# Performance work log

Hardware: AMD Instinct MI355X
Metric: run time of the kernel (lower is better)

The kernel has to match this reference:

```python
import jax, jax.numpy as jnp
import numpy as np

IN_SHAPE = (128, 128, 128)   # (d, w, h)
RES_SCALE = 1.5
SCAN_RANGE = 11.0
PROJ_NUM = 4
SPACING = np.array([1.0, 1.0, 1.0])
OUT_SHAPE = (256, 256)
BATCH = 2


def _make_grids():
    # Faithful numpy port of proj_layer._project_grid_multi (precomputed buffers).
    d, w, h = IN_SHAPE
    p = PROJ_NUM
    half = SCAN_RANGE / 2.0
    poses = np.zeros((p, 3))
    poses[:, 1] = 3.0
    poses[:, 0] = np.tan(np.linspace(-half, half, p) / 180.0 * np.pi) * 3.0
    poses[:, 2] = np.linspace(-0.2, 0.2, p)
    emi = poses * w                                  # emitter positions, (p,3)
    res_d, res_h = int(d * RES_SCALE), int(h * RES_SCALE)
    Nvec = np.array([0.0, 1.0, 0.0])
    P0 = np.linspace(0, w - 1, w)[:, None] * np.array([[0.0, 1.0, 0.0]])  # (w,3)
    lin_x = np.linspace(-res_d / 2, res_d / 2 - 1, res_d)
    lin_y = np.linspace(-res_h / 2, res_h / 2 - 1, res_h)
    gx, gy = np.meshgrid(lin_x, lin_y, indexing='ij')
    I = np.stack([gx, np.zeros_like(gx), gy], axis=-1)   # (rd,rh,3) detector plane
    I = I[None] - emi[:, None, None, :]                  # (p,rd,rh,3) ray dirs
    dxr = I / I[..., 1:2]
    In = I / np.linalg.norm(I, axis=3, keepdims=True)
    dxr = np.linalg.norm(dxr * SPACING[None, None, None, :], axis=3)  # (p,rd,rh) step length
    inv_IN = 1.0 / (In @ Nvec)                           # (p,rd,rh)
    PN = (P0[None] - emi[:, None, :]) @ Nvec             # (p,w)
    T = inv_IN[..., None] * PN[:, None, None, :]         # (p,rd,rh,w) ray params
    grid = In[..., None, :] * T[..., None] + emi[:, None, None, None, :]  # (p,rd,rh,w,3)
    gn = np.empty_like(grid)
    gn[..., 0] = grid[..., 0] / d * 2.0
    gn[..., 1] = grid[..., 1] / w * 2.0 - 1.0
    gn[..., 2] = grid[..., 2] / h * 2.0
    gn = gn[..., ::-1]  # torch.flip(grid, [4]) -> grid_sample (x,y,z) order
    return np.ascontiguousarray(gn).astype(np.float32), dxr.astype(np.float32)


def setup_inputs() -> dict:
    key = jax.random.key(0)
    x = jax.random.normal(key, (BATCH,) + IN_SHAPE, dtype=jnp.float32)
    g, dxr = _make_grids()
    return {"x": x, "grids": jnp.asarray(g), "dx": jnp.asarray(dxr)}


def _trilinear_gather(vol, coords):
    # vol: (b, D, H, W); coords: (N,3) normalized [-1,1], (x,y,z) -> (W,H,D)
    # F.grid_sample(mode='bilinear', padding_mode='zeros', align_corners=True)
    b, D, H, W = vol.shape
    ix = (coords[:, 0] + 1.0) * 0.5 * (W - 1)
    iy = (coords[:, 1] + 1.0) * 0.5 * (H - 1)
    iz = (coords[:, 2] + 1.0) * 0.5 * (D - 1)
    x0, y0, z0 = jnp.floor(ix), jnp.floor(iy), jnp.floor(iz)
    fx, fy, fz = ix - x0, iy - y0, iz - z0
    volf = vol.reshape(b, -1)
    out = jnp.zeros((b, coords.shape[0]), vol.dtype)
    for dz in (0, 1):
        wz = fz if dz else 1.0 - fz
        zi = z0 + dz
        for dy in (0, 1):
            wy = fy if dy else 1.0 - fy
            yi = y0 + dy
            for dxx in (0, 1):
                wx = fx if dxx else 1.0 - fx
                xi = x0 + dxx
                valid = ((xi >= 0) & (xi <= W - 1) & (yi >= 0) & (yi <= H - 1)
                         & (zi >= 0) & (zi <= D - 1))
                idx = ((jnp.clip(zi, 0, D - 1).astype(jnp.int32) * H
                        + jnp.clip(yi, 0, H - 1).astype(jnp.int32)) * W
                       + jnp.clip(xi, 0, W - 1).astype(jnp.int32))
                wgt = jnp.where(valid, wx * wy * wz, 0.0)
                out = out + volf[:, idx] * wgt[None, :]
    return out


def _nearest_resize(t, out_hw):
    # F.interpolate(mode='nearest'): src = floor(dst * in / out)
    b, c, H, W = t.shape
    oh, ow = out_hw
    hi = jnp.minimum((jnp.arange(oh) * H) // oh, H - 1)
    wi = jnp.minimum((jnp.arange(ow) * W) // ow, W - 1)
    return t[:, :, hi][:, :, :, wi]


def reference(x, grids, dx):
    p, rd, rh, w = grids.shape[:4]
    b = x.shape[0]
    coords = grids.reshape(-1, 3)                       # (p*rd*rh*w, 3)
    samples = _trilinear_gather(x, coords).reshape(b, p, rd, rh, w)
    x_proj = samples.sum(axis=4) * dx[None]             # ray-sum projection
    return _nearest_resize(x_proj, OUT_SHAPE)
```

## Files before the change

kernel.cpp:

```cpp
#include <hip/hip_runtime.h>
#include <hip/hip_bf16.h>

#define PNUM 4
#define RD   192
#define RH   192
#define OHH  256
#define OWW  256
#define NB   2
#define ROWS (PNUM * RD * RH)
#define VOL  (128 * 128 * 128)

typedef float        vf4 __attribute__((ext_vector_type(4)));
typedef float        vf2 __attribute__((ext_vector_type(2)));
typedef unsigned int vu2 __attribute__((ext_vector_type(2)));
typedef unsigned int vu4 __attribute__((ext_vector_type(4)));

__device__ __forceinline__ unsigned int bf16_bits(float f) {
    __hip_bfloat16 h = __float2bfloat16(f);
    return (unsigned int)__hip_bfloat16_raw(h).x;
}
__device__ __forceinline__ float hi_bits_f(unsigned int u) {
    u &= 0xffff0000u;
    return __builtin_bit_cast(float, u);
}
__device__ __forceinline__ float lo_bits_f(unsigned int u) {
    u <<= 16;
    return __builtin_bit_cast(float, u);
}


__global__ __launch_bounds__(256) void ray_setup_kernel(
    const float* __restrict__ grids,
    float* __restrict__ rayp,
    float* __restrict__ zp)
{
    const int ray = (int)(blockIdx.x * 256 + threadIdx.x);
    const float* g = grids + (size_t)ray * 384;
    const vf4 L0 = *(const vf4*)g;
    const vf4 L1 = *(const vf4*)(g + 192);
    vf2 r;
    r.x = (L0.x + 1.f) * 63.5f;
    r.y = (L1.x - L0.x) * 0.9921875f;
    *(vf2*)(rayp + (size_t)ray * 2) = r;
    if ((ray % RH) == 0) {
        vf2 z;
        z.x = (L0.z + 1.f) * 63.5f;
        z.y = (L1.z - L0.z) * 0.9921875f;
        *(vf2*)(zp + (size_t)(ray / RH) * 2) = z;
    }
}

__global__ __launch_bounds__(256) void ycomb_kernel(
    const float* __restrict__ x,
    vu2* __restrict__ ycomb)
{
    const int i  = (int)(blockIdx.x * 256 + threadIdx.x);
    const int w  = i >> 14;
    const int z  = (i >> 7) & 127;
    const int xc = i & 127;

    const float WY0 = (float)w * 0.0078125f;
    const float WY1 = 1.f - WY0;
    const int   rm  = (w > 0) ? (w - 1) : 0;

    const int b0 = (z * 128 + rm) * 128;
    const int b1 = (z * 128 + w) * 128;
    const int x1 = (xc < 127) ? (xc + 1) : 127;

    const float a0 = fmaf(WY0, x[b0 + xc],       WY1 * x[b1 + xc]);
    const float a1 = fmaf(WY0, x[VOL + b0 + xc], WY1 * x[VOL + b1 + xc]);
    const float c0 = fmaf(WY0, x[b0 + x1],       WY1 * x[b1 + x1]);
    const float c1 = fmaf(WY0, x[VOL + b0 + x1], WY1 * x[VOL + b1 + x1]);

    vu2 q;
    q.x = bf16_bits(a0) | (bf16_bits(a1) << 16);
    q.y = bf16_bits(c0) | (bf16_bits(c1) << 16);
    ycomb[i] = q;
}

__global__ __launch_bounds__(256) void proj_kernel(
    const vu2*  __restrict__ ycomb,
    const float* __restrict__ rayp,
    const float* __restrict__ zp,
    float* __restrict__ part)
{
    __shared__ __align__(16) vu2 lds[2][8][2][128];

    const int orig = (int)blockIdx.x;
    const int rdp  = (orig & 7) * (PNUM * RD / 8) + (orig >> 3);

    const int tid  = (int)threadIdx.x;
    const int wv   = tid >> 6;
    const int lane = tid & 63;

    const vf2 zv = *(const vf2*)(zp + (size_t)rdp * 2);

    const int  ray   = rdp * RH + wv * 64 + lane;
    const bool comp  = (wv < 3);
    vf2 xp = {0.f, 0.f};
    if (comp) xp = *(const vf2*)(rayp + (size_t)ray * 2);

    auto row_src = [&](int wb, int p) -> const vu4* {
        const int row = 4 * p + wv;
        const int wi  = row >> 1;
        const int zr  = row & 1;
        const int w   = wb + wi;
        const float iz = fmaf((float)w, zv.y, zv.x);
        const int   zb = (int)floorf(iz);
        const int   zi = zr ? min(max(zb + 1, 0), 127) : min(max(zb, 0), 127);
        return (const vu4*)(ycomb + ((size_t)w << 14) + ((size_t)zi << 7));
    };

    {
        const vu4 t0 = row_src(0, 0)[lane];
        const vu4 t1 = row_src(0, 1)[lane];
        const vu4 t2 = row_src(0, 2)[lane];
        const vu4 t3 = row_src(0, 3)[lane];
        ((vu4*)&lds[0][(4*0+wv)>>1][(4*0+wv)&1][0])[lane] = t0;
        ((vu4*)&lds[0][(4*1+wv)>>1][(4*1+wv)&1][0])[lane] = t1;
        ((vu4*)&lds[0][(4*2+wv)>>1][(4*2+wv)&1][0])[lane] = t2;
        ((vu4*)&lds[0][(4*3+wv)>>1][(4*3+wv)&1][0])[lane] = t3;
    }
    __syncthreads();

    float s0 = 0.f, s1 = 0.f;

    for (int c = 0; c < 16; ++c) {
        const int  buf = c & 1;
        const int  wb  = c * 8;
        const bool pre = (c < 15);

        vu4 t0, t1, t2, t3;
        if (pre) {
            t0 = row_src(wb + 8, 0)[lane];
            t1 = row_src(wb + 8, 1)[lane];
            t2 = row_src(wb + 8, 2)[lane];
            t3 = row_src(wb + 8, 3)[lane];
        }

        if (comp) {
#pragma unroll
            for (int wu = 0; wu < 8; ++wu) {
                const int   w  = wb + wu;
                const float wf = (float)w;
                const float ix = fmaf(wf, xp.y, xp.x);
                const float iz = fmaf(wf, zv.y, zv.x);

                const float xf = floorf(ix);
                const float fx = ix - xf;
                const int   xb = (int)xf;
                const int   xl = min(max(xb, 0), 126);
                const bool  inx = (xb >= 0) && (xb <= 126);
                const float WL = inx ? (1.f - fx) : ((xb == -1)  ? fx         : 0.f);
                const float WR = inx ? fx         : ((xb == 127) ? (1.f - fx) : 0.f);

                const float zf = floorf(iz);
                const float fz = iz - zf;
                const int   zb = (int)zf;
                const float WZ0 = (zb >= 0  && zb <= 127) ? (1.f - fz) : 0.f;
                const float WZ1 = (zb >= -1 && zb <= 126) ? fz         : 0.f;

                const vu2 q0 = lds[buf][wu][0][xl];
                const vu2 q1 = lds[buf][wu][1][xl];

                const float v00 = fmaf(WL, lo_bits_f(q0.x), WR * lo_bits_f(q0.y));
                const float v01 = fmaf(WL, hi_bits_f(q0.x), WR * hi_bits_f(q0.y));
                const float v10 = fmaf(WL, lo_bits_f(q1.x), WR * lo_bits_f(q1.y));
                const float v11 = fmaf(WL, hi_bits_f(q1.x), WR * hi_bits_f(q1.y));

                s0 = fmaf(WZ0, v00, fmaf(WZ1, v10, s0));
                s1 = fmaf(WZ0, v01, fmaf(WZ1, v11, s1));
            }
        }

        if (pre) {
            const int nb = buf ^ 1;
            ((vu4*)&lds[nb][(4*0+wv)>>1][(4*0+wv)&1][0])[lane] = t0;
            ((vu4*)&lds[nb][(4*1+wv)>>1][(4*1+wv)&1][0])[lane] = t1;
            ((vu4*)&lds[nb][(4*2+wv)>>1][(4*2+wv)&1][0])[lane] = t2;
            ((vu4*)&lds[nb][(4*3+wv)>>1][(4*3+wv)&1][0])[lane] = t3;
        }

        __syncthreads();
    }

    if (comp) {
        part[ray]        = s0;
        part[ROWS + ray] = s1;
    }
}


__global__ __launch_bounds__(256) void proj_rays_fb_kernel(
    const float* __restrict__ x,
    const float* __restrict__ grids,
    float* __restrict__ part)
{
    const int tid  = (int)(blockIdx.x * blockDim.x + threadIdx.x);
    const int wave = tid >> 6;
    const int lane = tid & 63;
    const int wcc  = wave & 3;
    const int rr   = wave >> 2;
    const int ray  = rr * 64 + lane;

    const float* g  = grids + (size_t)ray * 384 + wcc * 96;
    const float* v0 = x;
    const float* v1 = x + VOL;

    float s0 = 0.f, s1 = 0.f;
    for (int w0 = 0; w0 < 32; w0 += 16) {
        const vf4* gc = (const vf4*)(g + w0 * 3);
        float cf[48];
#pragma unroll
        for (int i = 0; i < 12; ++i) {
            const vf4 t = gc[i];
            cf[4*i+0] = t.x; cf[4*i+1] = t.y; cf[4*i+2] = t.z; cf[4*i+3] = t.w;
        }
#pragma unroll
        for (int w = 0; w < 16; ++w) {
            const float ix = (cf[3*w+0] + 1.f) * 63.5f;
            const float iy = (cf[3*w+1] + 1.f) * 63.5f;
            const float iz = (cf[3*w+2] + 1.f) * 63.5f;
            const float x0f = floorf(ix), y0f = floorf(iy), z0f = floorf(iz);
            const float fxx = ix - x0f, fyy = iy - y0f, fzz = iz - z0f;
            const float wx0 = (x0f >= 0.f && x0f <= 127.f) ? (1.f-fxx) : 0.f;
            const float wx1 = (x0f+1.f >= 0.f && x0f+1.f <= 127.f) ? fxx : 0.f;
            const float wy0 = (y0f >= 0.f && y0f <= 127.f) ? (1.f-fyy) : 0.f;
            const float wy1 = (y0f+1.f >= 0.f && y0f+1.f <= 127.f) ? fyy : 0.f;
            const float wz0 = (z0f >= 0.f && z0f <= 127.f) ? (1.f-fzz) : 0.f;
            const float wz1 = (z0f+1.f >= 0.f && z0f+1.f <= 127.f) ? fzz : 0.f;
            const int xi0 = (int)fminf(fmaxf(x0f,0.f),127.f);
            const int xi1 = (int)fminf(fmaxf(x0f+1.f,0.f),127.f);
            const int yi0 = (int)fminf(fmaxf(y0f,0.f),127.f);
            const int yi1 = (int)fminf(fmaxf(y0f+1.f,0.f),127.f);
            const int zi0 = (int)fminf(fmaxf(z0f,0.f),127.f);
            const int zi1 = (int)fminf(fmaxf(z0f+1.f,0.f),127.f);
            const int b00 = (zi0*128+yi0)*128, b01 = (zi0*128+yi1)*128;
            const int b10 = (zi1*128+yi0)*128, b11 = (zi1*128+yi1)*128;
            const float w000 = wz0*wy0*wx0, w001 = wz0*wy0*wx1;
            const float w010 = wz0*wy1*wx0, w011 = wz0*wy1*wx1;
            const float w100 = wz1*wy0*wx0, w101 = wz1*wy0*wx1;
            const float w110 = wz1*wy1*wx0, w111 = wz1*wy1*wx1;
            s0 += w000*v0[b00+xi0] + w001*v0[b00+xi1] + w010*v0[b01+xi0] + w011*v0[b01+xi1]
                + w100*v0[b10+xi0] + w101*v0[b10+xi1] + w110*v0[b11+xi0] + w111*v0[b11+xi1];
            s1 += w000*v1[b00+xi0] + w001*v1[b00+xi1] + w010*v1[b01+xi0] + w011*v1[b01+xi1]
                + w100*v1[b10+xi0] + w101*v1[b10+xi1] + w110*v1[b11+xi0] + w111*v1[b11+xi1];
        }
    }
    part[((size_t)wcc * NB + 0) * ROWS + ray] = s0;
    part[((size_t)wcc * NB + 1) * ROWS + ray] = s1;
}


__global__ __launch_bounds__(256) void resize_reduce_kernel(
    const float* __restrict__ part,
    const float* __restrict__ dx,
    float* __restrict__ out,
    int wsplit)
{
    const int idx = (int)(blockIdx.x * blockDim.x + threadIdx.x);
    const int ow = idx & (OWW - 1);
    const int oh = (idx >> 8) & (OHH - 1);
    const int bp = idx >> 16;
    const int b  = bp >> 2;
    const int p  = bp & 3;
    const int hi = (oh * 3) >> 2;
    const int wi = (ow * 3) >> 2;
    const int ray = (p * RD + hi) * RH + wi;

    float s = 0.f;
    for (int wcc = 0; wcc < wsplit; ++wcc)
        s += part[((size_t)wcc * NB + b) * ROWS + ray];
    out[idx] = s * dx[ray];
}

extern "C" void kernel_launch(void* const* d_in, const int* in_sizes, int n_in,
                              void* d_out, int out_size, void* d_ws, size_t ws_size,
                              hipStream_t stream) {
    const float* x     = (const float*)d_in[0];
    const float* grids = (const float*)d_in[1];
    const float* dx    = (const float*)d_in[2];
    float* out = (float*)d_out;
    char*  ws  = (char*)d_ws;

    const size_t YC_B   = (size_t)VOL * 8;
    const size_t RAYP_B = (size_t)ROWS * 2 * 4;
    const size_t ZP_B   = (size_t)PNUM * RD * 2 * 4;
    const size_t PART_B = (size_t)NB * ROWS * 4;
    const size_t NEED   = YC_B + RAYP_B + ZP_B + PART_B;

    if (ws_size >= NEED) {
        vu2*   ycomb = (vu2*)ws;
        float* rayp  = (float*)(ws + YC_B);
        float* zp    = (float*)(ws + YC_B + RAYP_B);
        float* part  = (float*)(ws + YC_B + RAYP_B + ZP_B);

        ray_setup_kernel<<<ROWS / 256, 256, 0, stream>>>(grids, rayp, zp);
        ycomb_kernel    <<<VOL / 256, 256, 0, stream>>>(x, ycomb);
        proj_kernel     <<<PNUM * RD, 256, 0, stream>>>(ycomb, rayp, zp, part);
        resize_reduce_kernel<<<(NB * PNUM * OHH * OWW) / 256, 256, 0, stream>>>(part, dx, out, 1);
    } else {
        float* part = (float*)ws;
        proj_rays_fb_kernel<<<ROWS * 4 / 256, 256, 0, stream>>>(x, grids, part);
        resize_reduce_kernel<<<(NB * PNUM * OHH * OWW) / 256, 256, 0, stream>>>(part, dx, out, 4);
    }
}
```

Measured before the change: 316.9 us.

## Split projection ray-march over four depth quarters with swizzled LDS staging

Result: faster. 309.3 us (-2.4%).

```diff
diff --git a/kernel.cpp b/kernel.cpp
--- a/kernel.cpp
+++ b/kernel.cpp
@@ -9,6 +9,7 @@
 #define NB   2
 #define ROWS (PNUM * RD * RH)
 #define VOL  (128 * 128 * 128)
+#define NRDP (PNUM * RD)
 
 typedef float        vf4 __attribute__((ext_vector_type(4)));
 typedef float        vf2 __attribute__((ext_vector_type(2)));
@@ -27,6 +28,10 @@
     u <<= 16;
     return __builtin_bit_cast(float, u);
 }
+__device__ __forceinline__ vf2 unpk(unsigned int u) {
+    vf2 r; r.x = lo_bits_f(u); r.y = hi_bits_f(u); return r;
+}
+__device__ __forceinline__ int swz(int e) { return e ^ ((e >> 4) & 7); }
 
 
 __global__ __launch_bounds__(256) void ray_setup_kernel(
@@ -84,10 +89,13 @@
     const float* __restrict__ zp,
     float* __restrict__ part)
 {
-    __shared__ __align__(16) vu2 lds[2][8][2][128];
+    __shared__ __align__(16) vu2 lds[2][4][2][128];
 
     const int orig = (int)blockIdx.x;
-    const int rdp  = (orig & 7) * (PNUM * RD / 8) + (orig >> 3);
+    const int bsw  = (orig & 7) * (3072 / 8) + (orig >> 3);
+    const int rdp  = bsw % NRDP;
+    const int q    = bsw / NRDP;
+    const int wq   = q * 32;
 
     const int tid  = (int)threadIdx.x;
     const int wv   = tid >> 6;
@@ -95,52 +103,56 @@
 
     const vf2 zv = *(const vf2*)(zp + (size_t)rdp * 2);
 
-    const int  ray   = rdp * RH + wv * 64 + lane;
-    const bool comp  = (wv < 3);
+    const int  ray  = rdp * RH + wv * 64 + lane;
+    const bool comp = (wv < 3);
     vf2 xp = {0.f, 0.f};
     if (comp) xp = *(const vf2*)(rayp + (size_t)ray * 2);
 
-    auto row_src = [&](int wb, int p) -> const vu4* {
-        const int row = 4 * p + wv;
-        const int wi  = row >> 1;
-        const int zr  = row & 1;
-        const int w   = wb + wi;
-        const float iz = fmaf((float)w, zv.y, zv.x);
-        const int   zb = (int)floorf(iz);
-        const int   zi = zr ? min(max(zb + 1, 0), 127) : min(max(zb, 0), 127);
-        return (const vu4*)(ycomb + ((size_t)w << 14) + ((size_t)zi << 7));
+    auto stage_load = [&](int wb, vu4& t0, vu4& t1) {
+#pragma unroll
+        for (int k = 0; k < 2; ++k) {
+            const int r  = 2 * wv + k;
+            const int wo = r >> 1;
+            const int zr = r & 1;
+            const int w  = wb + wo;
+            const float iz = fmaf((float)w, zv.y, zv.x);
+            const int   zb = (int)floorf(iz);
+            const int   zi = zr ? min(max(zb + 1, 0), 127) : min(max(zb, 0), 127);
+            const vu4 t = ((const vu4*)(ycomb + ((size_t)w << 14) + (zi << 7)))[lane];
+            if (k == 0) t0 = t; else t1 = t;
+        }
     };
-
-    {
-        const vu4 t0 = row_src(0, 0)[lane];
-        const vu4 t1 = row_src(0, 1)[lane];
-        const vu4 t2 = row_src(0, 2)[lane];
-        const vu4 t3 = row_src(0, 3)[lane];
-        ((vu4*)&lds[0][(4*0+wv)>>1][(4*0+wv)&1][0])[lane] = t0;
-        ((vu4*)&lds[0][(4*1+wv)>>1][(4*1+wv)&1][0])[lane] = t1;
-        ((vu4*)&lds[0][(4*2+wv)>>1][(4*2+wv)&1][0])[lane] = t2;
-        ((vu4*)&lds[0][(4*3+wv)>>1][(4*3+wv)&1][0])[lane] = t3;
-    }
+    auto stage_write = [&](int buf, const vu4& t0, const vu4& t1) {
+#pragma unroll
+        for (int k = 0; k < 2; ++k) {
+            const int r  = 2 * wv + k;
+            const int wo = r >> 1;
+            const int zr = r & 1;
+            const vu4 t  = k ? t1 : t0;
+            vu2 a; a.x = t.x; a.y = t.y;
+            vu2 b; b.x = t.z; b.y = t.w;
+            lds[buf][wo][zr][swz(2 * lane)]     = a;
+            lds[buf][wo][zr][swz(2 * lane + 1)] = b;
+        }
+    };
+
+    vu4 t0, t1;
+    stage_load(wq, t0, t1);
+    stage_write(0, t0, t1);
     __syncthreads();
 
-    float s0 = 0.f, s1 = 0.f;
-
-    for (int c = 0; c < 16; ++c) {
+    vf2 acc = {0.f, 0.f};
+
+    for (int c = 0; c < 8; ++c) {
         const int  buf = c & 1;
-        const int  wb  = c * 8;
-        const bool pre = (c < 15);
-
-        vu4 t0, t1, t2, t3;
-        if (pre) {
-            t0 = row_src(wb + 8, 0)[lane];
-            t1 = row_src(wb + 8, 1)[lane];
-            t2 = row_src(wb + 8, 2)[lane];
-            t3 = row_src(wb + 8, 3)[lane];
-        }
+        const int  wb  = wq + c * 4;
+        const bool pre = (c < 7);
+
+        if (pre) stage_load(wb + 4, t0, t1);
 
         if (comp) {
 #pragma unroll
-            for (int wu = 0; wu < 8; ++wu) {
+            for (int wu = 0; wu < 4; ++wu) {
                 const int   w  = wb + wu;
                 const float wf = (float)w;
                 const float ix = fmaf(wf, xp.y, xp.x);
@@ -160,33 +172,23 @@
                 const float WZ0 = (zb >= 0  && zb <= 127) ? (1.f - fz) : 0.f;
                 const float WZ1 = (zb >= -1 && zb <= 126) ? fz         : 0.f;
 
-                const vu2 q0 = lds[buf][wu][0][xl];
-                const vu2 q1 = lds[buf][wu][1][xl];
-
-                const float v00 = fmaf(WL, lo_bits_f(q0.x), WR * lo_bits_f(q0.y));
-                const float v01 = fmaf(WL, hi_bits_f(q0.x), WR * hi_bits_f(q0.y));
-                const float v10 = fmaf(WL, lo_bits_f(q1.x), WR * lo_bits_f(q1.y));
-                const float v11 = fmaf(WL, hi_bits_f(q1.x), WR * hi_bits_f(q1.y));
-
-                s0 = fmaf(WZ0, v00, fmaf(WZ1, v10, s0));
-                s1 = fmaf(WZ0, v01, fmaf(WZ1, v11, s1));
+                const int e = swz(xl);
+                const vu2 q0 = lds[buf][wu][0][e];
+                const vu2 q1 = lds[buf][wu][1][e];
+
+                const vf2 vx0 = WL * unpk(q0.x) + WR * unpk(q0.y);
+                const vf2 vx1 = WL * unpk(q1.x) + WR * unpk(q1.y);
+                acc = acc + WZ0 * vx0 + WZ1 * vx1;
             }
         }
 
-        if (pre) {
-            const int nb = buf ^ 1;
-            ((vu4*)&lds[nb][(4*0+wv)>>1][(4*0+wv)&1][0])[lane] = t0;
-            ((vu4*)&lds[nb][(4*1+wv)>>1][(4*1+wv)&1][0])[lane] = t1;
-            ((vu4*)&lds[nb][(4*2+wv)>>1][(4*2+wv)&1][0])[lane] = t2;
-            ((vu4*)&lds[nb][(4*3+wv)>>1][(4*3+wv)&1][0])[lane] = t3;
-        }
-
+        if (pre) stage_write(buf ^ 1, t0, t1);
         __syncthreads();
     }
 
     if (comp) {
-        part[ray]        = s0;
-        part[ROWS + ray] = s1;
+        part[((size_t)q * NB + 0) * ROWS + ray] = acc.x;
+        part[((size_t)q * NB + 1) * ROWS + ray] = acc.y;
     }
 }
 
@@ -285,8 +287,8 @@
 
     const size_t YC_B   = (size_t)VOL * 8;
     const size_t RAYP_B = (size_t)ROWS * 2 * 4;
-    const size_t ZP_B   = (size_t)PNUM * RD * 2 * 4;
-    const size_t PART_B = (size_t)NB * ROWS * 4;
+    const size_t ZP_B   = (size_t)NRDP * 2 * 4;
+    const size_t PART_B = (size_t)4 * NB * ROWS * 4;
     const size_t NEED   = YC_B + RAYP_B + ZP_B + PART_B;
 
     if (ws_size >= NEED) {
@@ -297,8 +299,8 @@
 
         ray_setup_kernel<<<ROWS / 256, 256, 0, stream>>>(grids, rayp, zp);
         ycomb_kernel    <<<VOL / 256, 256, 0, stream>>>(x, ycomb);
-        proj_kernel     <<<PNUM * RD, 256, 0, stream>>>(ycomb, rayp, zp, part);
-        resize_reduce_kernel<<<(NB * PNUM * OHH * OWW) / 256, 256, 0, stream>>>(part, dx, out, 1);
+        proj_kernel     <<<4 * NRDP, 256, 0, stream>>>(ycomb, rayp, zp, part);
+        resize_reduce_kernel<<<(NB * PNUM * OHH * OWW) / 256, 256, 0, stream>>>(part, dx, out, 4);
     } else {
         float* part = (float*)ws;
         proj_rays_fb_kernel<<<ROWS * 4 / 256, 256, 0, stream>>>(x, grids, part);
```
